# Optimization experiments

Hardware: AMD Instinct MI355X
Metric: run time of the kernel (lower is better)

The kernel has to match this reference:

```python
import jax, jax.numpy as jnp
import numpy as np

DH = 5.0       # spatial grid spacing
DT = 0.002     # time step
C  = 2200.0    # wave speed


def setup_inputs() -> dict:
    key = jax.random.key(0)
    # (N, C=1, T, H, W) wavefield snapshots
    inputs = jax.random.normal(key, (8, 1, 64, 256, 256), dtype=jnp.float32)
    return {"inputs": inputs}


def reference(inputs):
    # Effective conv weight is (1,1,3,3,3): single-channel 3x3x3 stencils.
    # padding=(0,1,1): valid along depth (time), zero-pad 1 along H and W.
    u = inputs[:, 0]  # (N, T, H, W)
    up = jnp.pad(u, ((0, 0), (0, 0), (1, 1), (1, 1)))  # zero-pad H, W
    c0 = up[:, 1:-1, 1:-1, 1:-1]  # center tap, (N, T-2, H, W)
    inv_dh2 = 1.0 / (DH * DH)
    inv_dt2 = 1.0 / (DT * DT)
    # [1,-2,1] along W (conv_x kernel)
    u_dxdx = (up[:, 1:-1, 1:-1, :-2] - 2.0 * c0 + up[:, 1:-1, 1:-1, 2:]) * inv_dh2
    # [1,-2,1] along H (conv_y kernel)
    u_dydy = (up[:, 1:-1, :-2, 1:-1] - 2.0 * c0 + up[:, 1:-1, 2:, 1:-1]) * inv_dh2
    # [1,-2,1] along T (conv_z kernel, valid)
    u_dtdt = (up[:, :-2, 1:-1, 1:-1] - 2.0 * c0 + up[:, 2:, 1:-1, 1:-1]) * inv_dt2
    residuals = u_dxdx + u_dydy - u_dtdt * (1.0 / (C * C))
    # torch.norm -> Frobenius norm over all elements
    return jnp.sqrt(jnp.sum(residuals * residuals))
```

## Files before the change

kernel.cpp:

```cpp
#include <hip/hip_runtime.h>
#include <math.h>

#define B_    8
#define T_    64
#define NY_   256
#define NX_   256
#define PS_   (NY_ * NX_)

#define YB_     4
#define NSTRIP  (NY_ / YB_)
#define TCHUNKS 8
#define NWAVES  (B_ * NSTRIP * TCHUNKS)
#define NTHREADS 256
#define NBLOCKS  (NWAVES / 4)

__device__ __forceinline__ float4 loadf4(const float* p) { return *(const float4*)p; }

template <int LEN>
__device__ __forceinline__ float strip_accum(const float* __restrict__ u,
                                             int b, int ys, int t0, int lane) {
    const float a   = 0.04f;
    const float kdt = 250000.0f / 4840000.0f;
    const float k2  = 2.0f * kdt - 4.0f * a;

    const int y0 = ys * YB_;
    const float m0 = (ys > 0)           ? 1.0f : 0.0f;
    const float m5 = (ys < NSTRIP - 1)  ? 1.0f : 0.0f;
    const float xl = (lane > 0)  ? 1.0f : 0.0f;
    const float xr = (lane < 63) ? 1.0f : 0.0f;

    int yoff[YB_ + 2];
    #pragma unroll
    for (int j = 0; j < YB_ + 2; ++j) {
        int y = y0 - 1 + j;
        y = y < 0 ? 0 : (y > NY_ - 1 ? NY_ - 1 : y);
        yoff[j] = y * NX_;
    }

    const float* pl = u + ((size_t)b * T_ + t0) * PS_ + lane * 4;

    float4 tm[YB_], c[YB_ + 2];
    #pragma unroll
    for (int i = 0; i < YB_; ++i) tm[i] = loadf4(pl + yoff[i + 1]);
    const float* p1 = pl + PS_;
    #pragma unroll
    for (int j = 0; j < YB_ + 2; ++j) c[j] = loadf4(p1 + yoff[j]);
    c[0].x *= m0; c[0].y *= m0; c[0].z *= m0; c[0].w *= m0;
    c[YB_+1].x *= m5; c[YB_+1].y *= m5; c[YB_+1].z *= m5; c[YB_+1].w *= m5;

    float acc = 0.0f;
    const float* pn = pl + 2 * PS_;
    #pragma unroll
    for (int k = 0; k < LEN; ++k) {
        float4 nn[YB_ + 2];
        #pragma unroll
        for (int j = 0; j < YB_ + 2; ++j) nn[j] = loadf4(pn + yoff[j]);
        nn[0].x *= m0; nn[0].y *= m0; nn[0].z *= m0; nn[0].w *= m0;
        nn[YB_+1].x *= m5; nn[YB_+1].y *= m5; nn[YB_+1].z *= m5; nn[YB_+1].w *= m5;

        #pragma unroll
        for (int i = 0; i < YB_; ++i) {
            float4 ctr = c[i + 1], up = c[i], dn = c[i + 2];
            float4 t = tm[i], nf = nn[i + 1];
            float cl = __shfl_up(ctr.w, 1, 64) * xl;
            float cr = __shfl_down(ctr.x, 1, 64) * xr;

            {
                float s2 = cl + ctr.y + up.x + dn.x;
                float r = fmaf(s2, a, fmaf(t.x + nf.x, -kdt, ctr.x * k2));
                acc = fmaf(r, r, acc);
            }
            {
                float s2 = ctr.x + ctr.z + up.y + dn.y;
                float r = fmaf(s2, a, fmaf(t.y + nf.y, -kdt, ctr.y * k2));
                acc = fmaf(r, r, acc);
            }
            {
                float s2 = ctr.y + ctr.w + up.z + dn.z;
                float r = fmaf(s2, a, fmaf(t.z + nf.z, -kdt, ctr.z * k2));
                acc = fmaf(r, r, acc);
            }
            {
                float s2 = ctr.z + cr + up.w + dn.w;
                float r = fmaf(s2, a, fmaf(t.w + nf.w, -kdt, ctr.w * k2));
                acc = fmaf(r, r, acc);
            }
        }

        #pragma unroll
        for (int i = 0; i < YB_; ++i) tm[i] = c[i + 1];
        #pragma unroll
        for (int j = 0; j < YB_ + 2; ++j) c[j] = nn[j];
        pn += PS_;
    }
    return acc;
}

__global__ __launch_bounds__(NTHREADS, 4)
void pinn_residual_partial(const float* __restrict__ u, float* __restrict__ partial) {
    const int lane = threadIdx.x & 63;
    const int w    = threadIdx.x >> 6;

    const int b     = blockIdx.x & 7;
    const int inner = blockIdx.x >> 3;
    const int wl    = inner * 4 + w;
    const int ys = wl & (NSTRIP - 1);
    const int tc = wl >> 6;
    const int t0 = tc * 8;

    float s;
    if (tc < TCHUNKS - 1) s = strip_accum<8>(u, b, ys, t0, lane);
    else                  s = strip_accum<6>(u, b, ys, t0, lane);

    #pragma unroll
    for (int off = 32; off > 0; off >>= 1)
        s += __shfl_down(s, off, 64);

    __shared__ float lds[NTHREADS / 64];
    if (lane == 0) lds[w] = s;
    __syncthreads();
    if (threadIdx.x == 0) {
        float bs = lds[0] + lds[1] + lds[2] + lds[3];
        partial[blockIdx.x] = bs;
    }
}

__global__ __launch_bounds__(NTHREADS)
void pinn_finalize(const float* __restrict__ partial, float* __restrict__ out) {
    float s = 0.0f;
    for (int i = threadIdx.x; i < NBLOCKS; i += NTHREADS)
        s += partial[i];
    #pragma unroll
    for (int off = 32; off > 0; off >>= 1)
        s += __shfl_down(s, off, 64);
    __shared__ float lds[NTHREADS / 64];
    int lane = threadIdx.x & 63;
    int wid  = threadIdx.x >> 6;
    if (lane == 0) lds[wid] = s;
    __syncthreads();
    if (threadIdx.x == 0) {
        float bs = 0.0f;
        #pragma unroll
        for (int q = 0; q < NTHREADS / 64; ++q) bs += lds[q];
        out[0] = sqrtf(bs);
    }
}

extern "C" void kernel_launch(void* const* d_in, const int* in_sizes, int n_in,
                              void* d_out, int out_size, void* d_ws, size_t ws_size,
                              hipStream_t stream) {
    const float* u = (const float*)d_in[0];
    float* partial = (float*)d_ws;
    float* out     = (float*)d_out;

    pinn_residual_partial<<<NBLOCKS, NTHREADS, 0, stream>>>(u, partial);
    pinn_finalize<<<1, NTHREADS, 0, stream>>>(partial, out);
}
```

Measured before the change: 31.68 us.

## Stage next time plane into LDS via async global_load_lds double buffering

Each block's four waves now cover a contiguous 16-row band and share its halo rows. The next time plane is staged into a double-buffered LDS tile with the async global_load_lds builtin and overlapped with compute. This cuts redundant halo loads from global memory and hides load latency. In exchange it adds a __syncthreads per time step and about 36KB of LDS per block, which limits occupancy. It also splits the launch into two kernels, one for full and one for tail time chunks.

```diff
diff --git a/kernel.cpp b/kernel.cpp
--- a/kernel.cpp
+++ b/kernel.cpp
@@ -8,55 +8,96 @@
 #define PS_   (NY_ * NX_)
 
 #define YB_     4
-#define NSTRIP  (NY_ / YB_)
+#define WPB_    4
+#define ROWS_   (WPB_ * YB_)
+#define HR_     (ROWS_ + 2)
 #define TCHUNKS 8
-#define NWAVES  (B_ * NSTRIP * TCHUNKS)
 #define NTHREADS 256
-#define NBLOCKS  (NWAVES / 4)
+#define YBLOCKS (NY_ / ROWS_)
+#define NBLOCKS (B_ * YBLOCKS * TCHUNKS)
 
 __device__ __forceinline__ float4 loadf4(const float* p) { return *(const float4*)p; }
 
+__device__ __forceinline__ void stage_plane(const float* __restrict__ plane,
+                                            float* __restrict__ dst ,
+                                            int Y0, int w, int lane) {
+    typedef __attribute__((address_space(1))) const unsigned int gu32;
+    typedef __attribute__((address_space(3))) unsigned int lu32;
+    #pragma unroll
+    for (int j = 0; j < 4; ++j) {
+        int r = w + 4 * j;
+        int y = Y0 - 1 + r;
+        y = y < 0 ? 0 : (y > NY_ - 1 ? NY_ - 1 : y);
+        const float* gp = plane + y * NX_ + lane * 4;
+        __builtin_amdgcn_global_load_lds((gu32*)gp, (lu32*)(dst + r * NX_), 16, 0, 0);
+    }
+    if (w < 2) {
+        int r = 16 + w;
+        int y = Y0 - 1 + r;
+        y = y > NY_ - 1 ? NY_ - 1 : y;
+        const float* gp = plane + y * NX_ + lane * 4;
+        __builtin_amdgcn_global_load_lds((gu32*)gp, (lu32*)(dst + r * NX_), 16, 0, 0);
+    }
+}
+
 template <int LEN>
-__device__ __forceinline__ float strip_accum(const float* __restrict__ u,
-                                             int b, int ys, int t0, int lane) {
+__global__ __launch_bounds__(NTHREADS, 4)
+void pinn_residual_partial(const float* __restrict__ u, float* __restrict__ partial,
+                           int tc_base) {
+    __shared__ float buf[2][HR_][NX_];
+
     const float a   = 0.04f;
     const float kdt = 250000.0f / 4840000.0f;
     const float k2  = 2.0f * kdt - 4.0f * a;
 
-    const int y0 = ys * YB_;
-    const float m0 = (ys > 0)           ? 1.0f : 0.0f;
-    const float m5 = (ys < NSTRIP - 1)  ? 1.0f : 0.0f;
+    const int lane = threadIdx.x & 63;
+    const int w    = threadIdx.x >> 6;
+
+    const int b     = blockIdx.x & 7;
+    const int inner = blockIdx.x >> 3;
+    const int yb    = inner & (YBLOCKS - 1);
+    const int tc    = tc_base + (inner >> 4);
+    const int t0    = tc * 8;
+    const int Y0    = yb * ROWS_;
+
+    const int yfirst = Y0 + 4 * w;
+    const float m0 = (yfirst > 0)          ? 1.0f : 0.0f;
+    const float m5 = (yfirst + 3 < NY_ - 1)? 1.0f : 0.0f;
     const float xl = (lane > 0)  ? 1.0f : 0.0f;
     const float xr = (lane < 63) ? 1.0f : 0.0f;
 
-    int yoff[YB_ + 2];
-    #pragma unroll
-    for (int j = 0; j < YB_ + 2; ++j) {
-        int y = y0 - 1 + j;
-        y = y < 0 ? 0 : (y > NY_ - 1 ? NY_ - 1 : y);
-        yoff[j] = y * NX_;
-    }
-
-    const float* pl = u + ((size_t)b * T_ + t0) * PS_ + lane * 4;
+    const float* plane0 = u + ((size_t)b * T_ + t0) * PS_;
 
     float4 tm[YB_], c[YB_ + 2];
     #pragma unroll
-    for (int i = 0; i < YB_; ++i) tm[i] = loadf4(pl + yoff[i + 1]);
-    const float* p1 = pl + PS_;
+    for (int i = 0; i < YB_; ++i)
+        tm[i] = loadf4(plane0 + (yfirst + i) * NX_ + lane * 4);
+    const float* plane1 = plane0 + PS_;
     #pragma unroll
-    for (int j = 0; j < YB_ + 2; ++j) c[j] = loadf4(p1 + yoff[j]);
+    for (int j = 0; j < YB_ + 2; ++j) {
+        int y = yfirst - 1 + j;
+        y = y < 0 ? 0 : (y > NY_ - 1 ? NY_ - 1 : y);
+        c[j] = loadf4(plane1 + y * NX_ + lane * 4);
+    }
     c[0].x *= m0; c[0].y *= m0; c[0].z *= m0; c[0].w *= m0;
-    c[YB_+1].x *= m5; c[YB_+1].y *= m5; c[YB_+1].z *= m5; c[YB_+1].w *= m5;
+    c[5].x *= m5; c[5].y *= m5; c[5].z *= m5; c[5].w *= m5;
+
+    stage_plane(plane0 + 2 * PS_, &buf[0][0][0], Y0, w, lane);
+    __syncthreads();
 
     float acc = 0.0f;
-    const float* pn = pl + 2 * PS_;
+    int cur = 0;
     #pragma unroll
     for (int k = 0; k < LEN; ++k) {
+        if (k + 1 < LEN)
+            stage_plane(plane0 + (size_t)(3 + k) * PS_, &buf[cur ^ 1][0][0], Y0, w, lane);
+
         float4 nn[YB_ + 2];
         #pragma unroll
-        for (int j = 0; j < YB_ + 2; ++j) nn[j] = loadf4(pn + yoff[j]);
+        for (int j = 0; j < YB_ + 2; ++j)
+            nn[j] = *(const float4*)&buf[cur][4 * w + j][lane * 4];
         nn[0].x *= m0; nn[0].y *= m0; nn[0].z *= m0; nn[0].w *= m0;
-        nn[YB_+1].x *= m5; nn[YB_+1].y *= m5; nn[YB_+1].z *= m5; nn[YB_+1].w *= m5;
+        nn[5].x *= m5; nn[5].y *= m5; nn[5].z *= m5; nn[5].w *= m5;
 
         #pragma unroll
         for (int i = 0; i < YB_; ++i) {
@@ -91,33 +132,19 @@
         for (int i = 0; i < YB_; ++i) tm[i] = c[i + 1];
         #pragma unroll
         for (int j = 0; j < YB_ + 2; ++j) c[j] = nn[j];
-        pn += PS_;
+
+        if (k + 1 < LEN) {
+            __syncthreads();
+            cur ^= 1;
+        }
     }
-    return acc;
-}
-
-__global__ __launch_bounds__(NTHREADS, 4)
-void pinn_residual_partial(const float* __restrict__ u, float* __restrict__ partial) {
-    const int lane = threadIdx.x & 63;
-    const int w    = threadIdx.x >> 6;
-
-    const int b     = blockIdx.x & 7;
-    const int inner = blockIdx.x >> 3;
-    const int wl    = inner * 4 + w;
-    const int ys = wl & (NSTRIP - 1);
-    const int tc = wl >> 6;
-    const int t0 = tc * 8;
-
-    float s;
-    if (tc < TCHUNKS - 1) s = strip_accum<8>(u, b, ys, t0, lane);
-    else                  s = strip_accum<6>(u, b, ys, t0, lane);
 
     #pragma unroll
     for (int off = 32; off > 0; off >>= 1)
-        s += __shfl_down(s, off, 64);
+        acc += __shfl_down(acc, off, 64);
 
-    __shared__ float lds[NTHREADS / 64];
-    if (lane == 0) lds[w] = s;
+    __shared__ float lds[WPB_];
+    if (lane == 0) lds[w] = acc;
     __syncthreads();
     if (threadIdx.x == 0) {
         float bs = lds[0] + lds[1] + lds[2] + lds[3];
@@ -125,10 +152,14 @@
     }
 }
 
+#define NB_MAIN (B_ * YBLOCKS * (TCHUNKS - 1))
+#define NB_TAIL (B_ * YBLOCKS)
+#define NPART   (NB_MAIN + NB_TAIL)
+
 __global__ __launch_bounds__(NTHREADS)
 void pinn_finalize(const float* __restrict__ partial, float* __restrict__ out) {
     float s = 0.0f;
-    for (int i = threadIdx.x; i < NBLOCKS; i += NTHREADS)
+    for (int i = threadIdx.x; i < NPART; i += NTHREADS)
         s += partial[i];
     #pragma unroll
     for (int off = 32; off > 0; off >>= 1)
@@ -153,6 +184,7 @@
     float* partial = (float*)d_ws;
     float* out     = (float*)d_out;
 
-    pinn_residual_partial<<<NBLOCKS, NTHREADS, 0, stream>>>(u, partial);
+    pinn_residual_partial<8><<<NB_MAIN, NTHREADS, 0, stream>>>(u, partial, 0);
+    pinn_residual_partial<6><<<NB_TAIL, NTHREADS, 0, stream>>>(u, partial + NB_MAIN, 7);
     pinn_finalize<<<1, NTHREADS, 0, stream>>>(partial, out);
 }
```

Result: slower. 37.16 us (+17.3%).
